# Optimization experiments

Measured on AMD Instinct MI355X. Metric: run time of the kernel, lower is better.

## Reference

```python
import jax, jax.numpy as jnp
import numpy as np

OUT = 7
N, C, HMAX, WMAX = 512, 256, 14, 14


def setup_inputs() -> dict:
    key = jax.random.key(0)
    k1, k2, k3 = jax.random.split(key, 3)
    rois = jax.random.normal(k1, (N, C, HMAX, WMAX), dtype=jnp.float32)
    # valid ROI sizes in [7, 14] (padded up to HMAX/WMAX)
    h = jax.random.randint(k2, (N,), 7, HMAX + 1, dtype=jnp.int32)
    w = jax.random.randint(k3, (N,), 7, WMAX + 1, dtype=jnp.int32)
    return {"rois": rois, "h": h, "w": w}


def _bin_mask(sizes, max_len):
    # sizes: [N] valid lengths. Returns [N, OUT, max_len] bool membership mask
    # matching nn.AdaptiveMaxPool2d: bin i covers [floor(i*L/OUT), ceil((i+1)*L/OUT))
    i = jnp.arange(OUT, dtype=jnp.int32)[None, :]          # [1, OUT]
    L = sizes[:, None]                                      # [N, 1]
    start = (i * L) // OUT                                  # [N, OUT]
    end = ((i + 1) * L + OUT - 1) // OUT                    # ceil, [N, OUT]
    r = jnp.arange(max_len, dtype=jnp.int32)[None, None, :]  # [1, 1, max_len]
    return (r >= start[:, :, None]) & (r < end[:, :, None])  # [N, OUT, max_len]


def reference(rois, h, w):
    neg = jnp.finfo(rois.dtype).min
    mh = _bin_mask(h, HMAX)  # [N, OUT, HMAX]
    mw = _bin_mask(w, WMAX)  # [N, OUT, WMAX]
    # max over rows per row-bin: [N, C, OUT, WMAX]
    rowp = jnp.max(jnp.where(mh[:, None, :, :, None], rois[:, :, None, :, :], neg), axis=3)
    # max over cols per col-bin: [N, C, OUT, OUT]
    out = jnp.max(jnp.where(mw[:, None, None, :, :], rowp[:, :, :, None, :], neg), axis=4)
    # original: torch.cat of per-ROI [C, OUT, OUT] along dim 0 -> [N*C, OUT, OUT]
    return out.reshape(N * C, OUT, OUT)
```

## Files before the change

### kernel.cpp

```cpp
#include <hip/hip_runtime.h>
#include <float.h>


constexpr int N_   = 512;
constexpr int C_   = 256;
constexpr int HMAX = 14;
constexpr int WMAX = 14;
constexpr int OUT  = 7;
constexpr int PLANE = HMAX * WMAX;
constexpr int P     = 16;
constexpr int NBLK  = (N_ * C_) / P;
constexpr int NOUT  = P * OUT * OUT;

__global__ __launch_bounds__(256) void roipool_kernel(
    const float* __restrict__ rois,
    const int*   __restrict__ h,
    const int*   __restrict__ w,
    float*       __restrict__ out)
{
    __shared__ float lds[P * PLANE];

    const int tid = threadIdx.x;
    const int blk = blockIdx.x;

    const int n  = blk >> 4;
    const int Lh = h[n];
    const int Lw = w[n];
    const int V  = (7 * Lh + 1) >> 1;

    {
        const float4* src = (const float4*)rois + (size_t)blk * (NOUT);
        float4* ldsv = (float4*)lds;
        int p = tid >> 4;
        int l = tid & 15;
        int base = p * 49;
        for (int v = l; v < V; v += 16)
            ldsv[base + v] = src[base + v];
    }
    __syncthreads();

    if (tid < 196) {
        float m[4];
        const int o0 = tid * 4;
        #pragma unroll
        for (int u = 0; u < 4; ++u) {
            int o = o0 + u;
            int p = o / 49;
            int q = o - p * 49;
            int i = q / 7;
            int j = q - i * 7;

            int th = i * Lh;
            int tw = j * Lw;
            int r1 = (th * 147) >> 10;
            int r3 = (((th + Lh + 6) * 147) >> 10) - 1;
            int r2 = min(r1 + 1, r3);
            int c1 = (tw * 147) >> 10;
            int c3 = (((tw + Lw + 6) * 147) >> 10) - 1;
            int c2 = min(c1 + 1, c3);

            const float* base = lds + p * PLANE;
            const float* row1 = base + r1 * WMAX;
            const float* row2 = base + r2 * WMAX;
            const float* row3 = base + r3 * WMAX;

            float v0 = fmaxf(fmaxf(row1[c1], row1[c2]), row1[c3]);
            float v1 = fmaxf(fmaxf(row2[c1], row2[c2]), row2[c3]);
            float v2 = fmaxf(fmaxf(row3[c1], row3[c2]), row3[c3]);
            m[u] = fmaxf(fmaxf(v0, v1), v2);
        }
        float4 res = make_float4(m[0], m[1], m[2], m[3]);
        ((float4*)out)[(size_t)blk * (NOUT / 4) + tid] = res;
    }
}

extern "C" void kernel_launch(void* const* d_in, const int* in_sizes, int n_in,
                              void* d_out, int out_size, void* d_ws, size_t ws_size,
                              hipStream_t stream)
{
    const float* rois = (const float*)d_in[0];
    const int*   h    = (const int*)d_in[1];
    const int*   w    = (const int*)d_in[2];
    float*       out  = (float*)d_out;

    roipool_kernel<<<NBLK, 256, 0, stream>>>(rois, h, w, out);
}
```

Measured before the change: 24.61 us.

## Compute one output row per thread with Lw-specialized column pooling and LDS-staged stores

Each of 112 threads now takes one output row (plane, i). It reduces the three source rows vertically with float2 LDS reads into a 14-wide register vector, then pools horizontally using templates specialized on Lw through a switch. Results go to an LDS staging buffer and are written out as coalesced float4 stores after a second barrier. This removes the redundant per-element index math and the scattered 9-load LDS gathers. In exchange it uses fewer active threads, adds a barrier and extra LDS, and may cause bank conflicts on the strided ostage writes.

```diff
diff --git a/kernel.cpp b/kernel.cpp
--- a/kernel.cpp
+++ b/kernel.cpp
@@ -4,13 +4,23 @@
 
 constexpr int N_   = 512;
 constexpr int C_   = 256;
-constexpr int HMAX = 14;
 constexpr int WMAX = 14;
 constexpr int OUT  = 7;
-constexpr int PLANE = HMAX * WMAX;
+constexpr int PLANE = 196;
 constexpr int P     = 16;
 constexpr int NBLK  = (N_ * C_) / P;
 constexpr int NOUT  = P * OUT * OUT;
+
+template<int LW>
+__device__ __forceinline__ void hpool(const float (&vm)[WMAX], float (&o)[OUT]) {
+    #pragma unroll
+    for (int j = 0; j < OUT; ++j) {
+        int c1 = (j * LW) / 7;
+        int c3 = ((j + 1) * LW + 6) / 7 - 1;
+        int c2 = (c1 + 1 < c3) ? c1 + 1 : c3;
+        o[j] = fmaxf(fmaxf(vm[c1], vm[c2]), vm[c3]);
+    }
+}
 
 __global__ __launch_bounds__(256) void roipool_kernel(
     const float* __restrict__ rois,
@@ -19,6 +29,7 @@
     float*       __restrict__ out)
 {
     __shared__ float lds[P * PLANE];
+    __shared__ float ostage[NOUT];
 
     const int tid = threadIdx.x;
     const int blk = blockIdx.x;
@@ -39,38 +50,48 @@
     }
     __syncthreads();
 
-    if (tid < 196) {
-        float m[4];
-        const int o0 = tid * 4;
+    if (tid < P * OUT) {
+        int p = tid / 7;
+        int i = tid - p * 7;
+
+        int th = i * Lh;
+        int r1 = th / 7;
+        int r3 = (th + Lh + 6) / 7 - 1;
+        int r2 = min(r1 + 1, r3);
+
+        const float2* a = (const float2*)(lds + p * PLANE + r1 * WMAX);
+        const float2* b = (const float2*)(lds + p * PLANE + r2 * WMAX);
+        const float2* c = (const float2*)(lds + p * PLANE + r3 * WMAX);
+
+        float vm[WMAX];
         #pragma unroll
-        for (int u = 0; u < 4; ++u) {
-            int o = o0 + u;
-            int p = o / 49;
-            int q = o - p * 49;
-            int i = q / 7;
-            int j = q - i * 7;
+        for (int k = 0; k < 7; ++k) {
+            float2 x = a[k], y = b[k], z = c[k];
+            vm[2 * k]     = fmaxf(fmaxf(x.x, y.x), z.x);
+            vm[2 * k + 1] = fmaxf(fmaxf(x.y, y.y), z.y);
+        }
 
-            int th = i * Lh;
-            int tw = j * Lw;
-            int r1 = (th * 147) >> 10;
-            int r3 = (((th + Lh + 6) * 147) >> 10) - 1;
-            int r2 = min(r1 + 1, r3);
-            int c1 = (tw * 147) >> 10;
-            int c3 = (((tw + Lw + 6) * 147) >> 10) - 1;
-            int c2 = min(c1 + 1, c3);
+        float o[OUT];
+        switch (Lw) {
+            case  7: hpool< 7>(vm, o); break;
+            case  8: hpool< 8>(vm, o); break;
+            case  9: hpool< 9>(vm, o); break;
+            case 10: hpool<10>(vm, o); break;
+            case 11: hpool<11>(vm, o); break;
+            case 12: hpool<12>(vm, o); break;
+            case 13: hpool<13>(vm, o); break;
+            default: hpool<14>(vm, o); break;
+        }
 
-            const float* base = lds + p * PLANE;
-            const float* row1 = base + r1 * WMAX;
-            const float* row2 = base + r2 * WMAX;
-            const float* row3 = base + r3 * WMAX;
+        float* os = ostage + tid * OUT;
+        #pragma unroll
+        for (int j = 0; j < OUT; ++j) os[j] = o[j];
+    }
+    __syncthreads();
 
-            float v0 = fmaxf(fmaxf(row1[c1], row1[c2]), row1[c3]);
-            float v1 = fmaxf(fmaxf(row2[c1], row2[c2]), row2[c3]);
-            float v2 = fmaxf(fmaxf(row3[c1], row3[c2]), row3[c3]);
-            m[u] = fmaxf(fmaxf(v0, v1), v2);
-        }
-        float4 res = make_float4(m[0], m[1], m[2], m[3]);
-        ((float4*)out)[(size_t)blk * (NOUT / 4) + tid] = res;
+    if (tid < NOUT / 4) {
+        float4 v = ((const float4*)ostage)[tid];
+        ((float4*)out)[(size_t)blk * (NOUT / 4) + tid] = v;
     }
 }
 
```

New measurement: 25.14 us. 2.1% more time.
